# Kernel tuning notes

Measured on AMD Instinct MI355X. Metric: run time of the kernel, lower is better.

## Reference

```python
import jax, jax.numpy as jnp
import numpy as np
from jax import lax

RHO = 1.0
L = 50

def _pbc_index(rho=RHO, L=L):
    # S = {(m,n) | |mn| <= rho*L//2, |m|<=L//2, |n|<=L//2}; rho*L//2 == 25.0 here
    thr = (rho * L) // 2
    idx = [(m, n)
           for m in range(-L // 2, L // 2 + 1)
           for n in range(-L // 2, L // 2 + 1)
           if abs(m * n) <= thr]
    return np.asarray(idx, dtype=np.int32)  # [T, 2], T = 449


def setup_inputs() -> dict:
    key = jax.random.key(0)
    k1, k2, k3, k4 = jax.random.split(key, 4)
    B, S, Nmodes = 8, 16384, 2
    T = _pbc_index().shape[0]  # 449
    return {
        "E_real": jax.random.normal(k1, (B, S, Nmodes), dtype=jnp.float32),
        "E_imag": jax.random.normal(k2, (B, S, Nmodes), dtype=jnp.float32),
        "C_real": jax.random.normal(k3, (4, T), dtype=jnp.float32) * 0.01,
        "C_imag": jax.random.normal(k4, (4, T), dtype=jnp.float32) * 0.01,
    }


def reference(E_real, E_imag, C_real, C_imag):
    idx = _pbc_index()
    m = jnp.asarray(idx[:, 0])
    n = jnp.asarray(idx[:, 1])
    E = E_real + 1j * E_imag                 # [B, S, 2] complex64
    C = (C_real + 1j * C_imag)[0]            # task_info=None -> row 0, [T]

    # O_k,i = E_k,i + sum_{m,n} (E_{k+n,i} E*_{k+m+n,i} + E_{k+n,-i} E*_{k+m+n,-i}) E_{k+m,i} C_{m,n}
    def body(acc, term):
        mi, ni, ci = term
        A = jnp.roll(E, ni, axis=-2) * jnp.conj(jnp.roll(E, mi + ni, axis=-2))
        A = A + jnp.roll(A, 1, axis=-1)      # cross-polarization term (Nmodes=2)
        return acc + A * jnp.roll(E, mi, axis=-2) * ci, None

    acc, _ = lax.scan(body, jnp.zeros_like(E), (m, n, C))
    Eo = E + acc                             # P = 1 (task_info=None), sqrt(P)**3 = 1
    return Eo[..., L:-L, :]                  # drop overlaps: [B, S-2L, 2]
```

## Files before the change

kernel.cpp:

```cpp
#include <hip/hip_runtime.h>


typedef float v2f __attribute__((ext_vector_type(2)));
typedef float v4f __attribute__((ext_vector_type(4)));

#define S_LEN 16384
#define SOUT  16284
#define BLK   512
#define NOUT  256
#define NE    356
#define NE2   178
#define ND    307
#define ND_AL 308
#define NDP   154

constexpr int LIMS[26] = {25,25,12,8,6,5,4,3,3,2,2,2,2,
                          1,1,1,1,1,1,1,1,1,1,1,1,1};
constexpr int TS[51] = {
      0,  3,  6,  9, 12, 15, 18, 21, 24, 27, 30, 33, 36,
     39, 44, 49, 54, 59, 66, 73, 82, 93,106,123,148,199,
    250,301,326,343,356,367,376,383,390,395,400,405,410,
    413,416,419,422,425,428,431,434,437,440,443,446};

__device__ __forceinline__ uint32_t pack_bf(float re, float im) {
    uint32_t r;
    asm("v_cvt_pk_bf16_f32 %0, %1, %2" : "=v"(r) : "v"(re), "v"(im));
    return r;
}
__device__ __forceinline__ v2f unpack_bf(uint32_t u) {
    union { uint32_t i; float f; } lo, hi;
    lo.i = u << 16;
    hi.i = u & 0xFFFF0000u;
    return (v2f){lo.f, hi.f};
}

template<int M>
__device__ __forceinline__ void convM4(
    const uint32_t* __restrict__ sDm, const v4f* __restrict__ sEp,
    int o0, const float* __restrict__ Cr0, const float* __restrict__ Ci0,
    float4& acc01, float4& acc23)
{
    constexpr int lim = LIMS[M];
    constexpr int tp  = TS[25 + M];
    constexpr int tn  = TS[25 - M];
    constexpr int A   = 25 + lim;

    v2f SxP[4] = {{0.f,0.f},{0.f,0.f},{0.f,0.f},{0.f,0.f}};
    v2f SyP[4] = {{0.f,0.f},{0.f,0.f},{0.f,0.f},{0.f,0.f}};
    v2f SxN[4] = {{0.f,0.f},{0.f,0.f},{0.f,0.f},{0.f,0.f}};
    v2f SyN[4] = {{0.f,0.f},{0.f,0.f},{0.f,0.f},{0.f,0.f}};

#define TAP4(d_, dd)                                                        \
    { _Pragma("unroll")                                                     \
      for (int r = 0; r < 4; ++r) {                                         \
        if (A + r - (d_) >= 0 && A + r - (d_) <= 2*lim) {                   \
            const float cx = Cr0[tp + A + r - (d_)];                        \
            const float cy = Ci0[tp + A + r - (d_)];                        \
            SxP[r] += cx * (dd);  SyP[r] += cy * (dd);                      \
        }                                                                   \
        if (A + M + r - (d_) >= 0 && A + M + r - (d_) <= 2*lim) {           \
            const float cx = Cr0[tn + A + M + r - (d_)];                    \
            const float cy = Ci0[tn + A + M + r - (d_)];                    \
            SxN[r] += cx * (dd);  SyN[r] += cy * (dd);                      \
        }                                                                   \
      } }
#define TAP4P(d_, dd)                                                       \
    { _Pragma("unroll")                                                     \
      for (int r = 0; r < 4; ++r) {                                         \
        if (A + r - (d_) >= 0 && A + r - (d_) <= 2*lim) {                   \
            const float cx = Cr0[tp + A + r - (d_)];                        \
            const float cy = Ci0[tp + A + r - (d_)];                        \
            SxP[r] += cx * (dd);  SyP[r] += cy * (dd);                      \
        }                                                                   \
      } }
#define TAP4N(d_, dd)                                                       \
    { _Pragma("unroll")                                                     \
      for (int r = 0; r < 4; ++r) {                                         \
        if (A + M + r - (d_) >= 0 && A + M + r - (d_) <= 2*lim) {           \
            const float cx = Cr0[tn + A + M + r - (d_)];                    \
            const float cy = Ci0[tn + A + M + r - (d_)];                    \
            SxN[r] += cx * (dd);  SyN[r] += cy * (dd);                      \
        }                                                                   \
      } }
#define QUAD(d0_, TAPM)                                                     \
    {                                                                       \
        uint4 u = *reinterpret_cast<const uint4*>(&sDm[o0 + (d0_)]);        \
        TAPM((d0_) + 0, unpack_bf(u.x))                                     \
        TAPM((d0_) + 1, unpack_bf(u.y))                                     \
        TAPM((d0_) + 2, unpack_bf(u.z))                                     \
        TAPM((d0_) + 3, unpack_bf(u.w))                                     \
    }

    if constexpr (M < 2*lim + 4) {
        constexpr int dlo = (25 - lim) & ~3;
        constexpr int dhi = 28 + lim + M;
        constexpr int NQ  = (dhi - dlo) / 4 + 1;
        #pragma unroll
        for (int q = 0; q < NQ; ++q)
            QUAD(dlo + 4*q, TAP4)
    } else {
        {
            constexpr int dlo = (25 - lim) & ~3;
            constexpr int dhi = 28 + lim;
            constexpr int NQ  = (dhi - dlo) / 4 + 1;
            #pragma unroll
            for (int q = 0; q < NQ; ++q)
                QUAD(dlo + 4*q, TAP4P)
        }
        {
            constexpr int dlo = (25 + M - lim) & ~3;
            constexpr int dhi = 28 + M + lim;
            constexpr int NQ  = (dhi - dlo) / 4 + 1;
            #pragma unroll
            for (int q = 0; q < NQ; ++q)
                QUAD(dlo + 4*q, TAP4N)
        }
    }
#undef QUAD
#undef TAP4
#undef TAP4P
#undef TAP4N

    #pragma unroll
    for (int r = 0; r < 4; ++r) {
        const float spr = SxP[r].x - SyP[r].y, spi = SxP[r].y + SyP[r].x;
        const float snr = SxN[r].x + SyN[r].y, sni = SyN[r].x - SxN[r].y;
        const int sp = o0 + 50 + r - M;
        const int sn = o0 + 50 + r + M;
        v4f ep = sEp[(sp >> 1) + ((sp & 1) ? NE2 : 0)];
        v4f en = sEp[(sn >> 1) + ((sn & 1) ? NE2 : 0)];
        const float c0 = spr*ep.x - spi*ep.y + snr*en.x - sni*en.y;
        const float c1 = spr*ep.z - spi*ep.w + snr*en.z - sni*en.w;
        if      (r == 0) { acc01.x += c0; acc01.y += c1; }
        else if (r == 1) { acc01.z += c0; acc01.w += c1; }
        else if (r == 2) { acc23.x += c0; acc23.y += c1; }
        else             { acc23.z += c0; acc23.w += c1; }
    }
}

__device__ __forceinline__ void conv04(
    const float* __restrict__ sD0p, const v4f* __restrict__ sEp,
    int o0, const float* __restrict__ Cr0, const float* __restrict__ Ci0,
    float4& acc01, float4& acc23)
{
    v2f s[4] = {{0.f,0.f},{0.f,0.f},{0.f,0.f},{0.f,0.f}};
    #pragma unroll
    for (int q = 0; q < 14; ++q) {
        const int d0 = 4*q;
        v4f w = *reinterpret_cast<const v4f*>(&sD0p[o0 + d0]);
        #pragma unroll
        for (int e = 0; e < 4; ++e) {
            const int d = d0 + e;
            const float dv = (e==0) ? w.x : (e==1) ? w.y : (e==2) ? w.z : w.w;
            #pragma unroll
            for (int r = 0; r < 4; ++r) {
                if (50 + r - d >= 0 && 50 + r - d <= 50) {
                    v2f cv = { Cr0[199 + 50 + r - d], Ci0[199 + 50 + r - d] };
                    s[r] += dv * cv;
                }
            }
        }
    }
    #pragma unroll
    for (int r = 0; r < 4; ++r) {
        const int sp = o0 + 50 + r;
        v4f e = sEp[(sp >> 1) + ((sp & 1) ? NE2 : 0)];
        const float c0 = s[r].x*e.x - s[r].y*e.y;
        const float c1 = s[r].x*e.z - s[r].y*e.w;
        if      (r == 0) { acc01.x += c0; acc01.y += c1; }
        else if (r == 1) { acc01.z += c0; acc01.w += c1; }
        else if (r == 2) { acc23.x += c0; acc23.y += c1; }
        else             { acc23.z += c0; acc23.w += c1; }
    }
}

__global__ __launch_bounds__(BLK, 4) void pbc_kernel(
    const float* __restrict__ Er, const float* __restrict__ Ei,
    const float* __restrict__ Cr, const float* __restrict__ Ci,
    float* __restrict__ out)
{
    __shared__ __align__(16) v4f      sEp[NE];
    __shared__ __align__(16) uint32_t sDbf[25 * ND_AL];
    __shared__ __align__(16) float    sD0[ND_AL];
    __shared__ __align__(16) float4   sAcc[7][64][2];

    const int b   = blockIdx.y;
    const int k0  = blockIdx.x * NOUT;
    const int tid = threadIdx.x;

    const float* erb = Er + (size_t)b * (S_LEN * 2);
    const float* eib = Ei + (size_t)b * (S_LEN * 2);
    if (tid < NE2) {
        const int i  = tid;
        const int kg = k0 + 2 * i;
        v4f rr = {0.f,0.f,0.f,0.f}, ii = {0.f,0.f,0.f,0.f};
        if (kg < S_LEN) {
            rr = *reinterpret_cast<const v4f*>(erb + 2 * kg);
            ii = *reinterpret_cast<const v4f*>(eib + 2 * kg);
        }
        sEp[i]       = (v4f){rr.x, ii.x, rr.y, ii.y};
        sEp[i + NE2] = (v4f){rr.z, ii.z, rr.w, ii.w};
    }
    __syncthreads();

    const int chunk = tid / NDP;
    const int xp    = tid - chunk * NDP;

#define D_ROW(mv)                                                           \
    {                                                                       \
        const int m_  = (mv);                                               \
        const int sb  = 2 * xp + 25 - m_;                                   \
        const int ib0 = (sb >> 1) + (sb & 1) * NE2;                         \
        const int ib1 = ((sb + 1) >> 1) + ((sb + 1) & 1) * NE2;             \
        v4f b0 = sEp[ib0], b1 = sEp[ib1];                                   \
        float gr0 = a0.x*b0.x + a0.y*b0.y + a0.z*b0.z + a0.w*b0.w;          \
        float gi0 = a0.y*b0.x - a0.x*b0.y + a0.w*b0.z - a0.z*b0.w;          \
        float gr1 = a1.x*b1.x + a1.y*b1.y + a1.z*b1.z + a1.w*b1.w;          \
        float gi1 = a1.y*b1.x - a1.x*b1.y + a1.w*b1.z - a1.z*b1.w;          \
        *reinterpret_cast<uint2*>(&sDbf[(m_ - 1) * ND_AL + 2 * xp]) =       \
            make_uint2(pack_bf(gr0, gi0), pack_bf(gr1, gi1));               \
    }

    if (chunk < 3) {
        v4f a0 = sEp[xp + 12 + NE2];
        v4f a1 = sEp[xp + 13];
        if (chunk == 0) {
            float d0 = a0.x*a0.x + a0.y*a0.y + a0.z*a0.z + a0.w*a0.w;
            float d1 = a1.x*a1.x + a1.y*a1.y + a1.z*a1.z + a1.w*a1.w;
            *reinterpret_cast<float2*>(&sD0[2 * xp]) = make_float2(d0, d1);
            #pragma unroll
            for (int m = 1; m <= 7; ++m) D_ROW(m)
        } else if (chunk == 1) {
            #pragma unroll
            for (int m = 8; m <= 16; ++m) D_ROW(m)
        } else {
            #pragma unroll
            for (int m = 17; m <= 25; ++m) D_ROW(m)
        }
    }
#undef D_ROW
    __syncthreads();

    const int g  = tid >> 6;
    const int t  = tid & 63;
    const int o0 = 4 * t;

    float4 acc01 = make_float4(0.f,0.f,0.f,0.f);
    float4 acc23 = make_float4(0.f,0.f,0.f,0.f);
#define DM(mm) (sDbf + ((mm) - 1) * ND_AL)
    if (g == 0) {
        conv04(sD0, sEp, o0, Cr, Ci, acc01, acc23);
        convM4<1>(DM(1), sEp, o0, Cr, Ci, acc01, acc23);
    } else if (g == 1) {
        convM4<2>(DM(2), sEp, o0, Cr, Ci, acc01, acc23);
        convM4<3>(DM(3), sEp, o0, Cr, Ci, acc01, acc23);
        convM4<4>(DM(4), sEp, o0, Cr, Ci, acc01, acc23);
    } else if (g == 2) {
        convM4<5>(DM(5), sEp, o0, Cr, Ci, acc01, acc23);
        convM4<6>(DM(6), sEp, o0, Cr, Ci, acc01, acc23);
        convM4<7>(DM(7), sEp, o0, Cr, Ci, acc01, acc23);
    } else if (g == 3) {
        convM4<8>(DM(8), sEp, o0, Cr, Ci, acc01, acc23);
        convM4<9>(DM(9), sEp, o0, Cr, Ci, acc01, acc23);
        convM4<10>(DM(10), sEp, o0, Cr, Ci, acc01, acc23);
    } else if (g == 4) {
        convM4<11>(DM(11), sEp, o0, Cr, Ci, acc01, acc23);
        convM4<12>(DM(12), sEp, o0, Cr, Ci, acc01, acc23);
        convM4<13>(DM(13), sEp, o0, Cr, Ci, acc01, acc23);
    } else if (g == 5) {
        convM4<14>(DM(14), sEp, o0, Cr, Ci, acc01, acc23);
        convM4<15>(DM(15), sEp, o0, Cr, Ci, acc01, acc23);
        convM4<16>(DM(16), sEp, o0, Cr, Ci, acc01, acc23);
        convM4<17>(DM(17), sEp, o0, Cr, Ci, acc01, acc23);
    } else if (g == 6) {
        convM4<18>(DM(18), sEp, o0, Cr, Ci, acc01, acc23);
        convM4<19>(DM(19), sEp, o0, Cr, Ci, acc01, acc23);
        convM4<20>(DM(20), sEp, o0, Cr, Ci, acc01, acc23);
        convM4<21>(DM(21), sEp, o0, Cr, Ci, acc01, acc23);
    } else {
        convM4<22>(DM(22), sEp, o0, Cr, Ci, acc01, acc23);
        convM4<23>(DM(23), sEp, o0, Cr, Ci, acc01, acc23);
        convM4<24>(DM(24), sEp, o0, Cr, Ci, acc01, acc23);
        convM4<25>(DM(25), sEp, o0, Cr, Ci, acc01, acc23);
    }
#undef DM
    if (g > 0) {
        sAcc[g - 1][t][0] = acc01;
        sAcc[g - 1][t][1] = acc23;
    }
    __syncthreads();

    if (tid < 64) {
        const int tt = tid;
        const int oo = 4 * tt;
        const int ko = k0 + oo;
        if (ko < SOUT) {
            float4 a01 = acc01, a23 = acc23;
            #pragma unroll
            for (int i = 0; i < 7; ++i) {
                float4 p0 = sAcc[i][tt][0], p1 = sAcc[i][tt][1];
                a01.x += p0.x; a01.y += p0.y; a01.z += p0.z; a01.w += p0.w;
                a23.x += p1.x; a23.y += p1.y; a23.z += p1.z; a23.w += p1.w;
            }
            v4f e0 = sEp[2*tt + 25];
            v4f e1 = sEp[2*tt + 25 + NE2];
            v4f e2 = sEp[2*tt + 26];
            v4f e3 = sEp[2*tt + 26 + NE2];
            float4 o0v, o1v;
            o0v.x = e0.x + a01.x;  o0v.y = e0.z + a01.y;
            o0v.z = e1.x + a01.z;  o0v.w = e1.z + a01.w;
            o1v.x = e2.x + a23.x;  o1v.y = e2.z + a23.y;
            o1v.z = e3.x + a23.z;  o1v.w = e3.z + a23.w;
            float* dst = out + ((size_t)b * SOUT + ko) * 2;
            *reinterpret_cast<float4*>(dst)     = o0v;
            *reinterpret_cast<float4*>(dst + 4) = o1v;
        }
    }
}

extern "C" void kernel_launch(void* const* d_in, const int* in_sizes, int n_in,
                              void* d_out, int out_size, void* d_ws, size_t ws_size,
                              hipStream_t stream) {
    const float* Er = (const float*)d_in[0];
    const float* Ei = (const float*)d_in[1];
    const float* Cr = (const float*)d_in[2];
    const float* Ci = (const float*)d_in[3];
    float* out = (float*)d_out;

    dim3 grid((SOUT + NOUT - 1) / NOUT, 8);
    pbc_kernel<<<grid, BLK, 0, stream>>>(Er, Ei, Cr, Ci, out);
}
```

Before: 15.37 us.

## Double block size to 1024 threads and rebalance m-row work across 16 waves

Raises the block to 1024 threads (16 wave groups) and splits the D-row precompute over 6 chunks instead of 3. The per-group convolution assignment is rebalanced so each wave handles one or two m values, weighted by per-m work. Cross-group reduction grows to 15 partials in shared memory. This aims to shorten the critical path per block by spreading work over more waves, at the cost of a larger reduction, more shared memory, and a possibly tighter register budget under launch_bounds(1024,8).

```diff
diff --git a/kernel.cpp b/kernel.cpp
--- a/kernel.cpp
+++ b/kernel.cpp
@@ -6,7 +6,7 @@
 
 #define S_LEN 16384
 #define SOUT  16284
-#define BLK   512
+#define BLK   1024
 #define NOUT  256
 #define NE    356
 #define NE2   178
@@ -174,7 +174,7 @@
     }
 }
 
-__global__ __launch_bounds__(BLK, 4) void pbc_kernel(
+__global__ __launch_bounds__(BLK, 8) void pbc_kernel(
     const float* __restrict__ Er, const float* __restrict__ Ei,
     const float* __restrict__ Cr, const float* __restrict__ Ci,
     float* __restrict__ out)
@@ -182,7 +182,7 @@
     __shared__ __align__(16) v4f      sEp[NE];
     __shared__ __align__(16) uint32_t sDbf[25 * ND_AL];
     __shared__ __align__(16) float    sD0[ND_AL];
-    __shared__ __align__(16) float4   sAcc[7][64][2];
+    __shared__ __align__(16) float4   sAcc[15][64][2];
 
     const int b   = blockIdx.y;
     const int k0  = blockIdx.x * NOUT;
@@ -221,7 +221,7 @@
             make_uint2(pack_bf(gr0, gi0), pack_bf(gr1, gi1));               \
     }
 
-    if (chunk < 3) {
+    if (chunk < 6) {
         v4f a0 = sEp[xp + 12 + NE2];
         v4f a1 = sEp[xp + 13];
         if (chunk == 0) {
@@ -229,13 +229,22 @@
             float d1 = a1.x*a1.x + a1.y*a1.y + a1.z*a1.z + a1.w*a1.w;
             *reinterpret_cast<float2*>(&sD0[2 * xp]) = make_float2(d0, d1);
             #pragma unroll
-            for (int m = 1; m <= 7; ++m) D_ROW(m)
+            for (int m = 1; m <= 4; ++m) D_ROW(m)
         } else if (chunk == 1) {
             #pragma unroll
-            for (int m = 8; m <= 16; ++m) D_ROW(m)
+            for (int m = 5; m <= 8; ++m) D_ROW(m)
+        } else if (chunk == 2) {
+            #pragma unroll
+            for (int m = 9; m <= 12; ++m) D_ROW(m)
+        } else if (chunk == 3) {
+            #pragma unroll
+            for (int m = 13; m <= 16; ++m) D_ROW(m)
+        } else if (chunk == 4) {
+            #pragma unroll
+            for (int m = 17; m <= 20; ++m) D_ROW(m)
         } else {
             #pragma unroll
-            for (int m = 17; m <= 25; ++m) D_ROW(m)
+            for (int m = 21; m <= 25; ++m) D_ROW(m)
         }
     }
 #undef D_ROW
@@ -248,41 +257,32 @@
     float4 acc01 = make_float4(0.f,0.f,0.f,0.f);
     float4 acc23 = make_float4(0.f,0.f,0.f,0.f);
 #define DM(mm) (sDbf + ((mm) - 1) * ND_AL)
-    if (g == 0) {
-        conv04(sD0, sEp, o0, Cr, Ci, acc01, acc23);
-        convM4<1>(DM(1), sEp, o0, Cr, Ci, acc01, acc23);
-    } else if (g == 1) {
-        convM4<2>(DM(2), sEp, o0, Cr, Ci, acc01, acc23);
-        convM4<3>(DM(3), sEp, o0, Cr, Ci, acc01, acc23);
-        convM4<4>(DM(4), sEp, o0, Cr, Ci, acc01, acc23);
-    } else if (g == 2) {
-        convM4<5>(DM(5), sEp, o0, Cr, Ci, acc01, acc23);
-        convM4<6>(DM(6), sEp, o0, Cr, Ci, acc01, acc23);
-        convM4<7>(DM(7), sEp, o0, Cr, Ci, acc01, acc23);
-    } else if (g == 3) {
-        convM4<8>(DM(8), sEp, o0, Cr, Ci, acc01, acc23);
-        convM4<9>(DM(9), sEp, o0, Cr, Ci, acc01, acc23);
-        convM4<10>(DM(10), sEp, o0, Cr, Ci, acc01, acc23);
-    } else if (g == 4) {
-        convM4<11>(DM(11), sEp, o0, Cr, Ci, acc01, acc23);
-        convM4<12>(DM(12), sEp, o0, Cr, Ci, acc01, acc23);
-        convM4<13>(DM(13), sEp, o0, Cr, Ci, acc01, acc23);
-    } else if (g == 5) {
-        convM4<14>(DM(14), sEp, o0, Cr, Ci, acc01, acc23);
-        convM4<15>(DM(15), sEp, o0, Cr, Ci, acc01, acc23);
-        convM4<16>(DM(16), sEp, o0, Cr, Ci, acc01, acc23);
-        convM4<17>(DM(17), sEp, o0, Cr, Ci, acc01, acc23);
-    } else if (g == 6) {
-        convM4<18>(DM(18), sEp, o0, Cr, Ci, acc01, acc23);
-        convM4<19>(DM(19), sEp, o0, Cr, Ci, acc01, acc23);
-        convM4<20>(DM(20), sEp, o0, Cr, Ci, acc01, acc23);
-        convM4<21>(DM(21), sEp, o0, Cr, Ci, acc01, acc23);
-    } else {
-        convM4<22>(DM(22), sEp, o0, Cr, Ci, acc01, acc23);
-        convM4<23>(DM(23), sEp, o0, Cr, Ci, acc01, acc23);
-        convM4<24>(DM(24), sEp, o0, Cr, Ci, acc01, acc23);
-        convM4<25>(DM(25), sEp, o0, Cr, Ci, acc01, acc23);
-    }
+    if      (g == 0)  { convM4<1>(DM(1), sEp, o0, Cr, Ci, acc01, acc23); }
+    else if (g == 1)  { conv04(sD0, sEp, o0, Cr, Ci, acc01, acc23); }
+    else if (g == 2)  { convM4<2>(DM(2), sEp, o0, Cr, Ci, acc01, acc23); }
+    else if (g == 3)  { convM4<3>(DM(3), sEp, o0, Cr, Ci, acc01, acc23); }
+    else if (g == 4)  { convM4<4>(DM(4), sEp, o0, Cr, Ci, acc01, acc23); }
+    else if (g == 5)  { convM4<12>(DM(12), sEp, o0, Cr, Ci, acc01, acc23); }
+    else if (g == 6)  { convM4<5>(DM(5),  sEp, o0, Cr, Ci, acc01, acc23);
+                        convM4<13>(DM(13), sEp, o0, Cr, Ci, acc01, acc23); }
+    else if (g == 7)  { convM4<6>(DM(6),  sEp, o0, Cr, Ci, acc01, acc23);
+                        convM4<14>(DM(14), sEp, o0, Cr, Ci, acc01, acc23); }
+    else if (g == 8)  { convM4<7>(DM(7),  sEp, o0, Cr, Ci, acc01, acc23);
+                        convM4<15>(DM(15), sEp, o0, Cr, Ci, acc01, acc23); }
+    else if (g == 9)  { convM4<8>(DM(8),  sEp, o0, Cr, Ci, acc01, acc23);
+                        convM4<16>(DM(16), sEp, o0, Cr, Ci, acc01, acc23); }
+    else if (g == 10) { convM4<9>(DM(9),  sEp, o0, Cr, Ci, acc01, acc23);
+                        convM4<17>(DM(17), sEp, o0, Cr, Ci, acc01, acc23); }
+    else if (g == 11) { convM4<10>(DM(10), sEp, o0, Cr, Ci, acc01, acc23);
+                        convM4<18>(DM(18), sEp, o0, Cr, Ci, acc01, acc23); }
+    else if (g == 12) { convM4<11>(DM(11), sEp, o0, Cr, Ci, acc01, acc23);
+                        convM4<19>(DM(19), sEp, o0, Cr, Ci, acc01, acc23); }
+    else if (g == 13) { convM4<20>(DM(20), sEp, o0, Cr, Ci, acc01, acc23);
+                        convM4<21>(DM(21), sEp, o0, Cr, Ci, acc01, acc23); }
+    else if (g == 14) { convM4<22>(DM(22), sEp, o0, Cr, Ci, acc01, acc23);
+                        convM4<23>(DM(23), sEp, o0, Cr, Ci, acc01, acc23); }
+    else              { convM4<24>(DM(24), sEp, o0, Cr, Ci, acc01, acc23);
+                        convM4<25>(DM(25), sEp, o0, Cr, Ci, acc01, acc23); }
 #undef DM
     if (g > 0) {
         sAcc[g - 1][t][0] = acc01;
@@ -297,7 +297,7 @@
         if (ko < SOUT) {
             float4 a01 = acc01, a23 = acc23;
             #pragma unroll
-            for (int i = 0; i < 7; ++i) {
+            for (int i = 0; i < 15; ++i) {
                 float4 p0 = sAcc[i][tt][0], p1 = sAcc[i][tt][1];
                 a01.x += p0.x; a01.y += p0.y; a01.z += p0.z; a01.w += p0.w;
                 a23.x += p1.x; a23.y += p1.y; a23.z += p1.z; a23.w += p1.w;
```

Result: slower. 17.30 us (+12.5%).
